# Optimization experiments

Measured on AMD Instinct MI355X. Metric: run time of the kernel, lower is better.

## Reference

```python
import jax, jax.numpy as jnp
import numpy as np

EPS = 1e-8  # torch cosine_similarity norm clamp
K = 5       # retrieval_k


def setup_inputs() -> dict:
    key = jax.random.key(0)
    ks = jax.random.split(key, 10)
    B, M, D, H = 256, 200000, 384, 512
    return {
        "query": jax.random.normal(ks[0], (B, D), jnp.float32),
        "memory_vectors": jax.random.normal(ks[1], (M, D), jnp.float32),
        "coords": jax.random.normal(ks[2], (M, 2), jnp.float32),
        "spatial_weights": jax.random.normal(ks[3], (H, 2), jnp.float32),
        "W_ih": jax.random.normal(ks[4], (H, D), jnp.float32) * 0.05,
        "b_ih": jax.random.normal(ks[5], (H,), jnp.float32) * 0.05,
        "W_hh": jax.random.normal(ks[6], (H, H), jnp.float32) * 0.05,
        "b_hh": jax.random.normal(ks[7], (H,), jnp.float32) * 0.05,
        "gate_W": jax.random.normal(ks[8], (H, D), jnp.float32) * 0.05,
        "gate_b": jax.random.normal(ks[9], (H,), jnp.float32) * 0.05,
    }


def reference(query, memory_vectors, coords, spatial_weights,
              W_ih, b_ih, W_hh, b_hh, gate_W, gate_b):
    B = query.shape[0]
    H = W_hh.shape[0]

    # spatial_activation: 1 / (1 + ||coords - mean(spatial_weights)||)
    center = spatial_weights.mean(axis=0)                       # [2]
    dists = jnp.linalg.norm(coords - center, axis=1)            # [M]
    activations = 1.0 / (1.0 + dists)                           # [M]

    # cosine similarity query vs all memories, plus spatial activation bias
    qn = query / jnp.clip(jnp.linalg.norm(query, axis=1, keepdims=True), EPS)
    mn = memory_vectors / jnp.clip(jnp.linalg.norm(memory_vectors, axis=1, keepdims=True), EPS)
    total_sim = qn @ mn.T + activations[None, :]                # [B, M]

    # top-k retrieval (sorted descending, like torch.topk)
    _, topk_idx = jax.lax.top_k(total_sim, K)                   # [B, K]
    retrieved = memory_vectors[topk_idx]                        # [B, K, D]

    # contextualize: tanh RNN over [query, retrieved_1..K]
    inputs = jnp.concatenate([query[:, None, :], retrieved], axis=1)  # [B, K+1, D]
    x_proj = jnp.einsum('btd,hd->bth', inputs, W_ih) + b_ih           # [B, K+1, H]

    def step(h, xp_t):  # h: [B,H], xp_t: [B,H]
        h = jnp.tanh(xp_t + h @ W_hh.T + b_hh)
        return h, None

    h0 = jnp.zeros((B, H), query.dtype)
    h, _ = jax.lax.scan(step, h0, jnp.swapaxes(x_proj, 0, 1))   # final h: [B, H]

    gate = jax.nn.sigmoid(query @ gate_W.T + gate_b)            # [B, H]
    projected_query = query @ W_ih.T + b_ih                     # [B, H]
    return gate * h + (1.0 - gate) * projected_query
```

## Files before the change

### kernel.cpp

```cpp
#include <hip/hip_runtime.h>
#include <math.h>

#define EPSC 1e-8f
#define TOPK 5

typedef _Float16 half8_t __attribute__((ext_vector_type(8)));
typedef float f32x4 __attribute__((ext_vector_type(4)));

__device__ __forceinline__ bool better(float va, int ia, float vb, int ib) {
    return (va > vb) || (va == vb && ia < ib);
}

__global__ void k_center(const float* __restrict__ sw, int H, float* __restrict__ center) {
    int tid = threadIdx.x;
    float sx = 0.f, sy = 0.f;
    for (int r = tid; r < H; r += 64) { sx += sw[2 * r]; sy += sw[2 * r + 1]; }
    for (int o = 32; o > 0; o >>= 1) { sx += __shfl_down(sx, o); sy += __shfl_down(sy, o); }
    if (tid == 0) { center[0] = sx / (float)H; center[1] = sy / (float)H; }
}

__global__ void k_qprep(const float* __restrict__ q, _Float16* __restrict__ Aglob, int B, int D) {
    int b = blockIdx.x;
    int tid = threadIdx.x;
    const int KCH = D >> 5;
    const int PS = 16 * KCH * 512;
    float ss = 0.f;
    for (int d = tid; d < D; d += 128) { float v = q[(size_t)b * D + d]; ss = fmaf(v, v, ss); }
    for (int o = 32; o > 0; o >>= 1) ss += __shfl_down(ss, o);
    __shared__ float w2[2];
    if ((tid & 63) == 0) w2[tid >> 6] = ss;
    __syncthreads();
    float inv = 1.f / fmaxf(sqrtf(w2[0] + w2[1]), EPSC);
    int qt = b >> 4, nl = b & 15;
    for (int d = tid; d < D; d += 128) {
        float v = q[(size_t)b * D + d] * inv;
        _Float16 hi = (_Float16)v;
        _Float16 lo = (_Float16)(v - (float)hi);
        int kc = d >> 5, r = d & 31, quad = r >> 3, j = r & 7;
        int idx = (qt * KCH + kc) * 512 + (quad * 16 + nl) * 8 + j;
        Aglob[idx] = hi;
        Aglob[PS + idx] = lo;
    }
}

__launch_bounds__(256, 2)
__global__ void k_sim_topk(const _Float16* __restrict__ Aglob, const float* __restrict__ mem,
                           const float* __restrict__ coords, const float* __restrict__ center,
                           float* __restrict__ candV, int* __restrict__ candI,
                           int M, int D) {
    __shared__ __align__(16) char smem[71168];
    _Float16* Ah = (_Float16*)smem;
    _Float16* Al = Ah + 8192;
    _Float16* Bh = Al + 8192;
    _Float16* Bl = Bh + 2048;
    float* Cs = (float*)smem;
    float* ssbuf = (float*)(smem + 69632);
    float* colinv = ssbuf + 256;
    float* colact = colinv + 64;

    const int tid = threadIdx.x;
    const int lane = tid & 63, w = tid >> 6;
    const int nB = tid >> 2, qB = tid & 3;
    const int KCH = D >> 5;
    const int PS = 16 * KCH * 512;
    const int n0 = blockIdx.x * 128;
    const float cx = center[0], cy = center[1];

    float lv[TOPK]; int li[TOPK];
#pragma unroll
    for (int k = 0; k < TOPK; ++k) { lv[k] = -INFINITY; li[k] = 0x7fffffff; }

    for (int ch = 0; ch < 2; ++ch) {
        const int base = n0 + ch * 64;
        f32x4 acc[4][4];
#pragma unroll
        for (int rt = 0; rt < 4; ++rt)
#pragma unroll
            for (int ct = 0; ct < 4; ++ct) acc[rt][ct] = (f32x4){0.f, 0.f, 0.f, 0.f};
        float ss = 0.f;
        const int brow = base + nB;
        const bool bvalid = brow < M;

        for (int kc = 0; kc < KCH; ++kc) {
            __syncthreads();
#pragma unroll
            for (int i = 0; i < 8; ++i) {
                int u = tid + i * 256;
                int p = u >> 10, rem = u & 1023, qt = rem >> 6, t = rem & 63;
                *(float4*)(smem + (size_t)u * 16) =
                    *(const float4*)(Aglob + (size_t)p * PS + (qt * KCH + kc) * 512 + t * 8);
            }
            {
                half8_t hv, lov;
                float vv[8];
                if (bvalid) {
                    const float* src = mem + (size_t)brow * D + kc * 32 + qB * 8;
                    float4 v0 = *(const float4*)src;
                    float4 v1 = *(const float4*)(src + 4);
                    vv[0] = v0.x; vv[1] = v0.y; vv[2] = v0.z; vv[3] = v0.w;
                    vv[4] = v1.x; vv[5] = v1.y; vv[6] = v1.z; vv[7] = v1.w;
                } else {
#pragma unroll
                    for (int j = 0; j < 8; ++j) vv[j] = 0.f;
                }
#pragma unroll
                for (int j = 0; j < 8; ++j) {
                    ss = fmaf(vv[j], vv[j], ss);
                    _Float16 h = (_Float16)vv[j];
                    hv[j] = h;
                    lov[j] = (_Float16)(vv[j] - (float)h);
                }
                int ct = nB >> 4, nl = nB & 15;
                int off = (ct * 64 + qB * 16 + nl) * 8;
                *(half8_t*)(Bh + off) = hv;
                *(half8_t*)(Bl + off) = lov;
            }
            __syncthreads();
            half8_t ah[4], al[4], bh[4], bl[4];
#pragma unroll
            for (int rt = 0; rt < 4; ++rt) {
                int qt = w * 4 + rt;
                ah[rt] = *(half8_t*)(Ah + qt * 512 + lane * 8);
                al[rt] = *(half8_t*)(Al + qt * 512 + lane * 8);
            }
#pragma unroll
            for (int ct = 0; ct < 4; ++ct) {
                bh[ct] = *(half8_t*)(Bh + (ct * 64 + lane) * 8);
                bl[ct] = *(half8_t*)(Bl + (ct * 64 + lane) * 8);
            }
#pragma unroll
            for (int rt = 0; rt < 4; ++rt)
#pragma unroll
                for (int ct = 0; ct < 4; ++ct) {
                    acc[rt][ct] = __builtin_amdgcn_mfma_f32_16x16x32_f16(ah[rt], bh[ct], acc[rt][ct], 0, 0, 0);
                    acc[rt][ct] = __builtin_amdgcn_mfma_f32_16x16x32_f16(ah[rt], bl[ct], acc[rt][ct], 0, 0, 0);
                    acc[rt][ct] = __builtin_amdgcn_mfma_f32_16x16x32_f16(al[rt], bh[ct], acc[rt][ct], 0, 0, 0);
                }
        }
        ssbuf[tid] = ss;
        __syncthreads();
        if (tid < 64) {
            float s = ssbuf[tid * 4] + ssbuf[tid * 4 + 1] + ssbuf[tid * 4 + 2] + ssbuf[tid * 4 + 3];
            colinv[tid] = 1.f / fmaxf(sqrtf(s), EPSC);
            int m = base + tid;
            float act = -INFINITY;
            if (m < M) {
                float dx = coords[2 * (size_t)m] - cx;
                float dy = coords[2 * (size_t)m + 1] - cy;
                act = 1.f / (1.f + sqrtf(dx * dx + dy * dy));
            }
            colact[tid] = act;
        }
        __syncthreads();
        float* Cw = Cs + w * (64 * 68);
        const int quad = lane >> 4, c15 = lane & 15;
#pragma unroll
        for (int rt = 0; rt < 4; ++rt)
#pragma unroll
            for (int ct = 0; ct < 4; ++ct) {
                int c = ct * 16 + c15;
                float inv = colinv[c], act = colact[c];
#pragma unroll
                for (int i = 0; i < 4; ++i) {
                    int row = rt * 16 + quad * 4 + i;
                    Cw[row * 68 + c] = fmaf(acc[rt][ct][i], inv, act);
                }
            }
        for (int j = 0; j < 64; ++j) {
            int c = (j + lane) & 63;
            float v = Cw[lane * 68 + c];
            int gi = base + c;
            if (better(v, gi, lv[4], li[4])) {
                lv[4] = v; li[4] = gi;
#pragma unroll
                for (int p = 4; p > 0; --p) {
                    if (better(lv[p], li[p], lv[p - 1], li[p - 1])) {
                        float tv = lv[p]; lv[p] = lv[p - 1]; lv[p - 1] = tv;
                        int ti = li[p]; li[p] = li[p - 1]; li[p - 1] = ti;
                    }
                }
            }
        }
        __syncthreads();
    }
    size_t cb = ((size_t)blockIdx.x * 256 + (w * 64 + lane)) * TOPK;
#pragma unroll
    for (int k = 0; k < TOPK; ++k) { candV[cb + k] = lv[k]; candI[cb + k] = li[k]; }
}

__global__ void k_merge(const float* __restrict__ candV, const int* __restrict__ candI,
                        int ntiles, int B, int* __restrict__ topk) {
    int b = blockIdx.x;
    int tid = threadIdx.x;
    float lv[TOPK]; int li[TOPK];
#pragma unroll
    for (int k = 0; k < TOPK; ++k) { lv[k] = -INFINITY; li[k] = 0x7fffffff; }
    for (int t = tid; t < ntiles; t += 256) {
        size_t base = ((size_t)t * B + b) * TOPK;
#pragma unroll
        for (int k = 0; k < TOPK; ++k) {
            float v = candV[base + k]; int gi = candI[base + k];
            if (better(v, gi, lv[4], li[4])) {
                lv[4] = v; li[4] = gi;
#pragma unroll
                for (int p = 4; p > 0; --p) {
                    if (better(lv[p], li[p], lv[p - 1], li[p - 1])) {
                        float tv = lv[p]; lv[p] = lv[p - 1]; lv[p - 1] = tv;
                        int ti = li[p]; li[p] = li[p - 1]; li[p - 1] = ti;
                    }
                }
            }
        }
    }
    __shared__ float sv[256 * TOPK];
    __shared__ int si[256 * TOPK];
#pragma unroll
    for (int k = 0; k < TOPK; ++k) { sv[tid * TOPK + k] = lv[k]; si[tid * TOPK + k] = li[k]; }
    __syncthreads();
    __shared__ float rv[256];
    __shared__ int ri[256], rp[256];
    for (int round = 0; round < TOPK; ++round) {
        float bv = -INFINITY; int bi = 0x7fffffff, bp = -1;
        for (int p = tid; p < 256 * TOPK; p += 256) {
            if (better(sv[p], si[p], bv, bi)) { bv = sv[p]; bi = si[p]; bp = p; }
        }
        rv[tid] = bv; ri[tid] = bi; rp[tid] = bp;
        __syncthreads();
        for (int st = 128; st > 0; st >>= 1) {
            if (tid < st) {
                if (better(rv[tid + st], ri[tid + st], rv[tid], ri[tid])) {
                    rv[tid] = rv[tid + st]; ri[tid] = ri[tid + st]; rp[tid] = rp[tid + st];
                }
            }
            __syncthreads();
        }
        if (tid == 0) {
            topk[b * TOPK + round] = ri[0];
            sv[rp[0]] = -INFINITY;
            si[rp[0]] = 0x7fffffff;
        }
        __syncthreads();
    }
}

__global__ void k_gather(const float* __restrict__ q, const float* __restrict__ mem,
                         const int* __restrict__ topk, float* __restrict__ inp, int D) {
    int r = blockIdx.x;
    int b = r / 6, t = r - b * 6;
    int tid = threadIdx.x;
    const float* src = (t == 0) ? (q + (size_t)b * D)
                                : (mem + (size_t)topk[b * TOPK + (t - 1)] * D);
    *(float4*)&inp[(size_t)r * D + tid * 4] = *(const float4*)&src[tid * 4];
}

__launch_bounds__(256)
__global__ void k_tail_gemm(const float* __restrict__ A, const float* __restrict__ W,
                            const float* __restrict__ bias, const float* __restrict__ addv,
                            int addv_stride, const float* __restrict__ gatep,
                            const float* __restrict__ xp0, int xp0_stride,
                            float* __restrict__ dst, int K, int ldc, int mode, int skipA) {
    __shared__ float As[16 * 68], Ws[16 * 68];
    const int r0 = blockIdx.x * 64, c0 = blockIdx.y * 64;
    const int tid = threadIdx.x;
    float acc[4][4];
#pragma unroll
    for (int i = 0; i < 4; ++i)
#pragma unroll
        for (int j = 0; j < 4; ++j) acc[i][j] = 0.f;
    if (!skipA) {
        const int lr = tid >> 2, lk4 = (tid & 3) * 4;
        for (int k0 = 0; k0 < K; k0 += 16) {
            __syncthreads();
            float4 av = *(const float4*)&A[(size_t)(r0 + lr) * K + k0 + lk4];
            float4 wv = *(const float4*)&W[(size_t)(c0 + lr) * K + k0 + lk4];
            As[(lk4 + 0) * 68 + lr] = av.x; As[(lk4 + 1) * 68 + lr] = av.y;
            As[(lk4 + 2) * 68 + lr] = av.z; As[(lk4 + 3) * 68 + lr] = av.w;
            Ws[(lk4 + 0) * 68 + lr] = wv.x; Ws[(lk4 + 1) * 68 + lr] = wv.y;
            Ws[(lk4 + 2) * 68 + lr] = wv.z; Ws[(lk4 + 3) * 68 + lr] = wv.w;
            __syncthreads();
#pragma unroll
            for (int k = 0; k < 16; ++k) {
                float4 a4 = *(float4*)&As[k * 68 + (tid >> 4) * 4];
                float4 b4 = *(float4*)&Ws[k * 68 + (tid & 15) * 4];
                float a[4] = {a4.x, a4.y, a4.z, a4.w};
                float bb[4] = {b4.x, b4.y, b4.z, b4.w};
#pragma unroll
                for (int i = 0; i < 4; ++i)
#pragma unroll
                    for (int j = 0; j < 4; ++j) acc[i][j] = fmaf(a[i], bb[j], acc[i][j]);
            }
        }
    }
    const int tr = (tid >> 4) * 4, tc = (tid & 15) * 4;
#pragma unroll
    for (int i = 0; i < 4; ++i) {
        int r = r0 + tr + i;
#pragma unroll
        for (int j = 0; j < 4; ++j) {
            int c = c0 + tc + j;
            float v = acc[i][j] + bias[c];
            if (mode >= 2) v += addv[(size_t)r * addv_stride + c];
            float res;
            if (mode == 0) res = v;
            else if (mode == 1) res = 1.f / (1.f + expf(-v));
            else if (mode == 2) res = tanhf(v);
            else {
                float hn = tanhf(v);
                float g = gatep[(size_t)r * ldc + c];
                res = g * hn + (1.f - g) * xp0[(size_t)r * xp0_stride + c];
            }
            dst[(size_t)r * ldc + c] = res;
        }
    }
}

extern "C" void kernel_launch(void* const* d_in, const int* in_sizes, int n_in,
                              void* d_out, int out_size, void* d_ws, size_t ws_size,
                              hipStream_t stream) {
    const float* query  = (const float*)d_in[0];
    const float* mem    = (const float*)d_in[1];
    const float* coords = (const float*)d_in[2];
    const float* sw     = (const float*)d_in[3];
    const float* W_ih   = (const float*)d_in[4];
    const float* b_ih   = (const float*)d_in[5];
    const float* W_hh   = (const float*)d_in[6];
    const float* b_hh   = (const float*)d_in[7];
    const float* gate_W = (const float*)d_in[8];
    const float* gate_b = (const float*)d_in[9];

    const int H = in_sizes[5];
    const int D = in_sizes[4] / H;
    const int B = in_sizes[0] / D;
    const int M = in_sizes[1] / D;
    const int KCH = D >> 5;
    const int ntiles = (M + 127) / 128;

    float* Wf = (float*)d_ws;
    size_t off = 0;
    _Float16* Aglob = (_Float16*)Wf;     off += (size_t)2 * 16 * KCH * 512 / 2;
    float* center = Wf + off; off += 4;
    float* candV  = Wf + off; off += (size_t)ntiles * B * TOPK;
    int*   candI  = (int*)(Wf + off); off += (size_t)ntiles * B * TOPK;
    int*   topk   = (int*)(Wf + off); off += B * TOPK;
    float* inp    = Wf + off; off += (size_t)B * 6 * D;
    float* xp     = Wf + off; off += (size_t)B * 6 * H;
    float* gate   = Wf + off; off += (size_t)B * H;
    float* hA     = Wf + off; off += (size_t)B * H;
    float* hB     = Wf + off; off += (size_t)B * H;

    k_center<<<1, 64, 0, stream>>>(sw, H, center);
    k_qprep<<<B, 128, 0, stream>>>(query, Aglob, B, D);
    k_sim_topk<<<ntiles, 256, 0, stream>>>(Aglob, mem, coords, center, candV, candI, M, D);
    k_merge<<<B, 256, 0, stream>>>(candV, candI, ntiles, B, topk);
    k_gather<<<B * 6, D / 4, 0, stream>>>(query, mem, topk, inp, D);
    k_tail_gemm<<<dim3(B * 6 / 64, H / 64), 256, 0, stream>>>(
        inp, W_ih, b_ih, nullptr, 0, nullptr, nullptr, 0, xp, D, H, 0, 0);
    k_tail_gemm<<<dim3(B / 64, H / 64), 256, 0, stream>>>(
        query, gate_W, gate_b, nullptr, 0, nullptr, nullptr, 0, gate, D, H, 1, 0);
    float* hprev = hA; float* hnext = hB;
    for (int t = 0; t <= TOPK; ++t) {
        int first = (t == 0), last = (t == TOPK);
        k_tail_gemm<<<dim3(B / 64, H / 64), 256, 0, stream>>>(
            hprev, W_hh, b_hh, xp + (size_t)t * H, 6 * H, gate, xp, 6 * H,
            last ? (float*)d_out : hnext, H, H, last ? 3 : 2, first);
        float* tmp = hprev; hprev = hnext; hnext = tmp;
    }
}
```

Baseline: 965.2 us.

## Stream query fragments from global, double-buffer B tile, shrink LDS for occupancy

```diff
diff --git a/kernel.cpp b/kernel.cpp
--- a/kernel.cpp
+++ b/kernel.cpp
@@ -9,6 +9,19 @@
 
 __device__ __forceinline__ bool better(float va, int ia, float vb, int ib) {
     return (va > vb) || (va == vb && ia < ib);
+}
+
+__device__ __forceinline__ void ins5(float v, int gi, float lv[TOPK], int li[TOPK]) {
+    if (better(v, gi, lv[4], li[4])) {
+        lv[4] = v; li[4] = gi;
+#pragma unroll
+        for (int p = 4; p > 0; --p) {
+            if (better(lv[p], li[p], lv[p - 1], li[p - 1])) {
+                float tv = lv[p]; lv[p] = lv[p - 1]; lv[p - 1] = tv;
+                int ti = li[p]; li[p] = li[p - 1]; li[p - 1] = ti;
+            }
+        }
+    }
 }
 
 __global__ void k_center(const float* __restrict__ sw, int H, float* __restrict__ center) {
@@ -22,8 +35,6 @@
 __global__ void k_qprep(const float* __restrict__ q, _Float16* __restrict__ Aglob, int B, int D) {
     int b = blockIdx.x;
     int tid = threadIdx.x;
-    const int KCH = D >> 5;
-    const int PS = 16 * KCH * 512;
     float ss = 0.f;
     for (int d = tid; d < D; d += 128) { float v = q[(size_t)b * D + d]; ss = fmaf(v, v, ss); }
     for (int o = 32; o > 0; o >>= 1) ss += __shfl_down(ss, o);
@@ -32,29 +43,44 @@
     __syncthreads();
     float inv = 1.f / fmaxf(sqrtf(w2[0] + w2[1]), EPSC);
     int qt = b >> 4, nl = b & 15;
+    int w = qt >> 2, rt = qt & 3;
     for (int d = tid; d < D; d += 128) {
         float v = q[(size_t)b * D + d] * inv;
         _Float16 hi = (_Float16)v;
         _Float16 lo = (_Float16)(v - (float)hi);
         int kc = d >> 5, r = d & 31, quad = r >> 3, j = r & 7;
-        int idx = (qt * KCH + kc) * 512 + (quad * 16 + nl) * 8 + j;
+        int lane = quad * 16 + nl;
+        size_t idx = (((size_t)kc * 4 + w) * 64 + lane) * 64 + rt * 16 + j;
         Aglob[idx] = hi;
-        Aglob[PS + idx] = lo;
-    }
-}
-
-__launch_bounds__(256, 2)
+        Aglob[idx + 8] = lo;
+    }
+}
+
+__device__ __forceinline__ void convwrite(float4 v0, float4 v1, _Float16* Bh, _Float16* Bl,
+                                          int off, float& ss) {
+    float vv[8] = {v0.x, v0.y, v0.z, v0.w, v1.x, v1.y, v1.z, v1.w};
+    half8_t hv, lov;
+#pragma unroll
+    for (int j = 0; j < 8; ++j) {
+        float f = vv[j];
+        ss = fmaf(f, f, ss);
+        _Float16 h = (_Float16)f;
+        hv[j] = h;
+        lov[j] = (_Float16)(f - (float)h);
+    }
+    *(half8_t*)(Bh + off) = hv;
+    *(half8_t*)(Bl + off) = lov;
+}
+
+__launch_bounds__(256, 3)
 __global__ void k_sim_topk(const _Float16* __restrict__ Aglob, const float* __restrict__ mem,
                            const float* __restrict__ coords, const float* __restrict__ center,
                            float* __restrict__ candV, int* __restrict__ candI,
                            int M, int D) {
-    __shared__ __align__(16) char smem[71168];
-    _Float16* Ah = (_Float16*)smem;
-    _Float16* Al = Ah + 8192;
-    _Float16* Bh = Al + 8192;
-    _Float16* Bl = Bh + 2048;
+    __shared__ __align__(16) char smem[36352];
+    _Float16* Bbuf = (_Float16*)smem;
     float* Cs = (float*)smem;
-    float* ssbuf = (float*)(smem + 69632);
+    float* ssbuf  = (float*)(smem + 34816);
     float* colinv = ssbuf + 256;
     float* colact = colinv + 64;
 
@@ -62,9 +88,11 @@
     const int lane = tid & 63, w = tid >> 6;
     const int nB = tid >> 2, qB = tid & 3;
     const int KCH = D >> 5;
-    const int PS = 16 * KCH * 512;
     const int n0 = blockIdx.x * 128;
     const float cx = center[0], cy = center[1];
+    const int quad = lane >> 4, c15 = lane & 15;
+    const int rr = lane & 31, hh = lane >> 5;
+    const int woff = ((nB >> 4) * 64 + qB * 16 + (nB & 15)) * 8;
 
     float lv[TOPK]; int li[TOPK];
 #pragma unroll
@@ -72,71 +100,61 @@
 
     for (int ch = 0; ch < 2; ++ch) {
         const int base = n0 + ch * 64;
+        const int brow = base + nB;
+        const bool bvalid = brow < M;
+        const float* mrow = mem + (size_t)brow * D;
         f32x4 acc[4][4];
 #pragma unroll
         for (int rt = 0; rt < 4; ++rt)
 #pragma unroll
             for (int ct = 0; ct < 4; ++ct) acc[rt][ct] = (f32x4){0.f, 0.f, 0.f, 0.f};
         float ss = 0.f;
-        const int brow = base + nB;
-        const bool bvalid = brow < M;
+
+        {
+            float4 v0 = {0.f, 0.f, 0.f, 0.f}, v1 = {0.f, 0.f, 0.f, 0.f};
+            if (bvalid) {
+                const float* p0 = mrow + qB * 8;
+                v0 = *(const float4*)p0;
+                v1 = *(const float4*)(p0 + 4);
+            }
+            convwrite(v0, v1, Bbuf, Bbuf + 2048, woff, ss);
+        }
 
         for (int kc = 0; kc < KCH; ++kc) {
+            const int p = kc & 1;
             __syncthreads();
-#pragma unroll
-            for (int i = 0; i < 8; ++i) {
-                int u = tid + i * 256;
-                int p = u >> 10, rem = u & 1023, qt = rem >> 6, t = rem & 63;
-                *(float4*)(smem + (size_t)u * 16) =
-                    *(const float4*)(Aglob + (size_t)p * PS + (qt * KCH + kc) * 512 + t * 8);
-            }
-            {
-                half8_t hv, lov;
-                float vv[8];
-                if (bvalid) {
-                    const float* src = mem + (size_t)brow * D + kc * 32 + qB * 8;
-                    float4 v0 = *(const float4*)src;
-                    float4 v1 = *(const float4*)(src + 4);
-                    vv[0] = v0.x; vv[1] = v0.y; vv[2] = v0.z; vv[3] = v0.w;
-                    vv[4] = v1.x; vv[5] = v1.y; vv[6] = v1.z; vv[7] = v1.w;
-                } else {
-#pragma unroll
-                    for (int j = 0; j < 8; ++j) vv[j] = 0.f;
+            half8_t ah[4], al[4];
+            const _Float16* aptr = Aglob + (((size_t)kc * 4 + w) * 64 + lane) * 64;
+#pragma unroll
+            for (int rt = 0; rt < 4; ++rt) {
+                ah[rt] = *(const half8_t*)(aptr + rt * 16);
+                al[rt] = *(const half8_t*)(aptr + rt * 16 + 8);
+            }
+            float4 n0v = {0.f, 0.f, 0.f, 0.f}, n1v = {0.f, 0.f, 0.f, 0.f};
+            if (kc + 1 < KCH && bvalid) {
+                const float* pn = mrow + (kc + 1) * 32 + qB * 8;
+                n0v = *(const float4*)pn;
+                n1v = *(const float4*)(pn + 4);
+            }
+            const _Float16* Bh = Bbuf + p * 4096;
+            const _Float16* Bl = Bh + 2048;
+#pragma unroll
+            for (int ct = 0; ct < 4; ++ct) {
+                half8_t bh = *(const half8_t*)(Bh + (ct * 64 + lane) * 8);
+                half8_t bl = *(const half8_t*)(Bl + (ct * 64 + lane) * 8);
+#pragma unroll
+                for (int rt = 0; rt < 4; ++rt) {
+                    acc[rt][ct] = __builtin_amdgcn_mfma_f32_16x16x32_f16(ah[rt], bh, acc[rt][ct], 0, 0, 0);
+                    acc[rt][ct] = __builtin_amdgcn_mfma_f32_16x16x32_f16(ah[rt], bl, acc[rt][ct], 0, 0, 0);
+                    acc[rt][ct] = __builtin_amdgcn_mfma_f32_16x16x32_f16(al[rt], bh, acc[rt][ct], 0, 0, 0);
                 }
-#pragma unroll
-                for (int j = 0; j < 8; ++j) {
-                    ss = fmaf(vv[j], vv[j], ss);
-                    _Float16 h = (_Float16)vv[j];
-                    hv[j] = h;
-                    lov[j] = (_Float16)(vv[j] - (float)h);
-                }
-                int ct = nB >> 4, nl = nB & 15;
-                int off = (ct * 64 + qB * 16 + nl) * 8;
-                *(half8_t*)(Bh + off) = hv;
-                *(half8_t*)(Bl + off) = lov;
-            }
-            __syncthreads();
-            half8_t ah[4], al[4], bh[4], bl[4];
-#pragma unroll
-            for (int rt = 0; rt < 4; ++rt) {
-                int qt = w * 4 + rt;
-                ah[rt] = *(half8_t*)(Ah + qt * 512 + lane * 8);
-                al[rt] = *(half8_t*)(Al + qt * 512 + lane * 8);
-            }
-#pragma unroll
-            for (int ct = 0; ct < 4; ++ct) {
-                bh[ct] = *(half8_t*)(Bh + (ct * 64 + lane) * 8);
-                bl[ct] = *(half8_t*)(Bl + (ct * 64 + lane) * 8);
-            }
-#pragma unroll
-            for (int rt = 0; rt < 4; ++rt)
-#pragma unroll
-                for (int ct = 0; ct < 4; ++ct) {
-                    acc[rt][ct] = __builtin_amdgcn_mfma_f32_16x16x32_f16(ah[rt], bh[ct], acc[rt][ct], 0, 0, 0);
-                    acc[rt][ct] = __builtin_amdgcn_mfma_f32_16x16x32_f16(ah[rt], bl[ct], acc[rt][ct], 0, 0, 0);
-                    acc[rt][ct] = __builtin_amdgcn_mfma_f32_16x16x32_f16(al[rt], bh[ct], acc[rt][ct], 0, 0, 0);
-                }
-        }
+            }
+            if (kc + 1 < KCH) {
+                _Float16* Bhn = Bbuf + (p ^ 1) * 4096;
+                convwrite(n0v, n1v, Bhn, Bhn + 2048, woff, ss);
+            }
+        }
+
         ssbuf[tid] = ss;
         __syncthreads();
         if (tid < 64) {
@@ -152,33 +170,42 @@
             colact[tid] = act;
         }
         __syncthreads();
-        float* Cw = Cs + w * (64 * 68);
-        const int quad = lane >> 4, c15 = lane & 15;
-#pragma unroll
-        for (int rt = 0; rt < 4; ++rt)
-#pragma unroll
-            for (int ct = 0; ct < 4; ++ct) {
-                int c = ct * 16 + c15;
-                float inv = colinv[c], act = colact[c];
-#pragma unroll
-                for (int i = 0; i < 4; ++i) {
-                    int row = rt * 16 + quad * 4 + i;
-                    Cw[row * 68 + c] = fmaf(acc[rt][ct][i], inv, act);
-                }
-            }
-        for (int j = 0; j < 64; ++j) {
-            int c = (j + lane) & 63;
-            float v = Cw[lane * 68 + c];
-            int gi = base + c;
-            if (better(v, gi, lv[4], li[4])) {
-                lv[4] = v; li[4] = gi;
-#pragma unroll
-                for (int p = 4; p > 0; --p) {
-                    if (better(lv[p], li[p], lv[p - 1], li[p - 1])) {
-                        float tv = lv[p]; lv[p] = lv[p - 1]; lv[p - 1] = tv;
-                        int ti = li[p]; li[p] = li[p - 1]; li[p - 1] = ti;
+
+        float* Cw = Cs + w * (32 * 68);
+#pragma unroll
+        for (int ps = 0; ps < 2; ++ps) {
+#pragma unroll
+            for (int rt2 = 0; rt2 < 2; ++rt2) {
+                const int rt = 2 * ps + rt2;
+#pragma unroll
+                for (int ct = 0; ct < 4; ++ct) {
+                    const int c = ct * 16 + c15;
+                    const float inv = colinv[c], act = colact[c];
+#pragma unroll
+                    for (int i = 0; i < 4; ++i) {
+                        Cw[(rt2 * 16 + quad * 4 + i) * 68 + c] = fmaf(acc[rt][ct][i], inv, act);
                     }
                 }
+            }
+            float tv5[TOPK]; int ti5[TOPK];
+#pragma unroll
+            for (int k = 0; k < TOPK; ++k) { tv5[k] = -INFINITY; ti5[k] = 0x7fffffff; }
+            const float* Crow = Cw + rr * 68 + hh * 32;
+            for (int j = 0; j < 32; ++j) {
+                const int cc = (j + lane) & 31;
+                ins5(Crow[cc], base + hh * 32 + cc, tv5, ti5);
+            }
+            float pv[TOPK]; int pi[TOPK];
+#pragma unroll
+            for (int k = 0; k < TOPK; ++k) {
+                pv[k] = __shfl_xor(tv5[k], 32);
+                pi[k] = __shfl_xor(ti5[k], 32);
+            }
+#pragma unroll
+            for (int k = 0; k < TOPK; ++k) ins5(pv[k], pi[k], tv5, ti5);
+            if (hh == ps) {
+#pragma unroll
+                for (int k = 0; k < TOPK; ++k) ins5(tv5[k], ti5[k], lv, li);
             }
         }
         __syncthreads();
```

Result: slower. 1.239 ms (+28.4%).
